# Performance work log

Hardware: AMD Instinct MI355X
Metric: run time of the kernel (lower is better)

## Reference

```python
import jax, jax.numpy as jnp
import numpy as np

N = 50000      # num nodes
E = 800000     # num edges
F_IN = 128     # CONFIG.FeatureLen()
H = 100        # conv1_hide
C = 16         # CONFIG.ClassNum()
LEAKY = 0.01


def setup_inputs() -> dict:
    key = jax.random.key(0)
    k = jax.random.split(key, 4)
    x = jax.random.normal(k[0], (N, F_IN), dtype=jnp.float32)
    edge_index = jax.random.randint(k[1], (2, E), 0, N, dtype=jnp.int32)
    W1 = jax.random.normal(k[2], (F_IN, H), dtype=jnp.float32) / np.sqrt(F_IN).astype(np.float32)
    b1 = jnp.zeros((H,), dtype=jnp.float32)
    W2 = jax.random.normal(k[3], (H, C), dtype=jnp.float32) / np.sqrt(H).astype(np.float32)
    b2 = jnp.zeros((C,), dtype=jnp.float32)
    return {"x": x, "W1": W1, "b1": b1, "W2": W2, "b2": b2, "edge_index": edge_index}


def _gcn_conv(x, W, b, src, dst):
    """PyG GCNConv: x' = D^{-1/2}(A+I)D^{-1/2} X W + b (symmetric norm, self-loops)."""
    x = x @ W  # transform first (smaller feature dim for propagation)
    loop = jnp.arange(N, dtype=src.dtype)
    s = jnp.concatenate([src, loop])  # sources (message senders)
    d = jnp.concatenate([dst, loop])  # targets (message receivers)
    deg = jax.ops.segment_sum(jnp.ones_like(d, dtype=x.dtype), d, num_segments=N)
    dinv = jnp.where(deg > 0, jax.lax.rsqrt(deg), 0.0)
    norm = dinv[s] * dinv[d]                      # [E+N]
    msg = x[s] * norm[:, None]                    # gather + scale
    out = jax.ops.segment_sum(msg, d, num_segments=N)  # scatter-add
    return out + b


def reference(x, W1, b1, W2, b2, edge_index):
    src, dst = edge_index[0], edge_index[1]
    h = _gcn_conv(x, W1, b1, src, dst)
    h = jax.nn.leaky_relu(h, negative_slope=LEAKY)
    # dropout is identity in eval mode (training=False)
    h = _gcn_conv(h, W2, b2, src, dst)
    return jax.nn.log_softmax(h, axis=1)
```

## Files before the change

kernel.cpp:

```cpp
#include <hip/hip_runtime.h>

#define F_IN 128
#define HDIM 100
#define HPAD 128
#define CDIM 16
#define CAP  64
#define BT_STRIDE 136
#define CHUNK 4096
#define KMAX 200
#define RCAP 64

static constexpr float LEAKY = 0.01f;

using short8  = __attribute__((ext_vector_type(8))) short;
using float4v = __attribute__((ext_vector_type(4))) float;
using float2v = __attribute__((ext_vector_type(2))) float;

__device__ __forceinline__ unsigned short f2bf(float f) {
    unsigned u = __float_as_uint(f);
    u += 0x7fffu + ((u >> 16) & 1u);
    return (unsigned short)(u >> 16);
}

__device__ __forceinline__ unsigned short f2h(float x) {
    union { unsigned short s; _Float16 f; } c;
    c.f = (_Float16)x;
    return c.s;
}

__device__ __forceinline__ float h2f(unsigned short u) {
    union { unsigned short s; _Float16 f; } c;
    c.s = u;
    return (float)c.f;
}


__global__ __launch_bounds__(256) void k_gemm1_p1(const float* __restrict__ x,
                                                  const float* __restrict__ W1,
                                                  unsigned char* __restrict__ y1f8,
                                                  const int* __restrict__ src,
                                                  const int* __restrict__ dst,
                                                  unsigned* __restrict__ bkt_edges,
                                                  int* __restrict__ cnt_arr,
                                                  int N, int E, int FB, int KBKT, int GB) {
    __shared__ union {
        unsigned short bt[F_IN * BT_STRIDE];
        struct { unsigned stage[CHUNK]; int cnt[KMAX]; } p1;
    } sm;
    int bx = blockIdx.x;
    int t = threadIdx.x;

    if (bx < FB) {
        unsigned* stage = sm.p1.stage;
        int* cnt = sm.p1.cnt;
        for (int i = t; i < KBKT; i += 256) cnt[i] = 0;
        __syncthreads();
        int e0 = bx * CHUNK, e1 = min(E, e0 + CHUNK);
        #pragma unroll 4
        for (int i = e0 + t; i < e1; i += 256) {
            int d = dst[i];
            unsigned pk = ((unsigned)d << 16) | (unsigned)src[i];
            atomicAdd(&cnt[d >> 8], 1);
            stage[i - e0] = pk;
        }
        __syncthreads();
        for (int i = t; i < KBKT; i += 256) cnt_arr[bx * KBKT + i] = cnt[i];
        __syncthreads();
        for (int i = t; i < KBKT; i += 256) cnt[i] = 0;
        __syncthreads();
        int m = e1 - e0;
        #pragma unroll 4
        for (int i = t; i < m; i += 256) {
            unsigned pk = stage[i];
            int b = pk >> 24;
            int pos = atomicAdd(&cnt[b], 1);
            if (pos < RCAP)
                bkt_edges[((size_t)b * FB + bx) * RCAP + pos] = pk;
        }
        return;
    }

    #pragma unroll 16
    for (int idx = t; idx < F_IN * HPAD; idx += 256) {
        int k = idx >> 7;
        int n = idx & 127;
        float v = (n < HDIM) ? W1[k * HDIM + n] : 0.f;
        sm.bt[n * BT_STRIDE + k] = f2bf(v);
    }
    __syncthreads();

    int wave = t >> 6, lane = t & 63;
    int Mtiles = (N + 15) >> 4;
    int m = lane & 15;
    int kq = lane >> 4;

    for (int tile = (bx - FB) * 4 + wave; tile < Mtiles; tile += 4 * GB) {
        int row0 = tile * 16;
        int arow = min(row0 + m, N - 1);
        const float* xrow = x + (size_t)arow * F_IN;

        short8 afrag[4];
        #pragma unroll
        for (int kt = 0; kt < 4; ++kt) {
            int kb = kt * 32 + kq * 8;
            float4 a0 = *(const float4*)(xrow + kb);
            float4 a1 = *(const float4*)(xrow + kb + 4);
            short8 f;
            f[0] = (short)f2bf(a0.x); f[1] = (short)f2bf(a0.y);
            f[2] = (short)f2bf(a0.z); f[3] = (short)f2bf(a0.w);
            f[4] = (short)f2bf(a1.x); f[5] = (short)f2bf(a1.y);
            f[6] = (short)f2bf(a1.z); f[7] = (short)f2bf(a1.w);
            afrag[kt] = f;
        }

        bool full = (row0 + 15 < N);
        #pragma unroll
        for (int ct = 0; ct < 8; ++ct) {
            float4v acc = {0.f, 0.f, 0.f, 0.f};
            #pragma unroll
            for (int kt = 0; kt < 4; ++kt) {
                short8 b = *(const short8*)&sm.bt[(ct * 16 + m) * BT_STRIDE + kt * 32 + kq * 8];
                acc = __builtin_amdgcn_mfma_f32_16x16x32_bf16(afrag[kt], b, acc, 0, 0, 0);
            }
            #pragma unroll
            for (int i = 0; i < 4; ++i) {
                int r = row0 + kq * 4 + i;
                int v8 = __builtin_amdgcn_cvt_pk_fp8_f32(acc[i], acc[i], 0, false);
                if (full || r < N)
                    y1f8[(size_t)r * HPAD + ct * 16 + m] = (unsigned char)(v8 & 0xff);
            }
        }
    }
}


__global__ __launch_bounds__(256) void k_p2(const unsigned* __restrict__ bkt_edges,
                                            const int* __restrict__ cnt_arr,
                                            int* __restrict__ deg,
                                            unsigned* __restrict__ slots,
                                            int N, int FB, int KBKT) {
    __shared__ int cur[256];
    int b = blockIdx.x, t = threadIdx.x;
    cur[t] = 0;
    __syncthreads();
    for (int fb = t; fb < FB; fb += 256) {
        int c = cnt_arr[fb * KBKT + b];
        size_t base = ((size_t)b * FB + fb) * RCAP;
        int j = 0;
        for (; j + 3 < c; j += 4) {
            uint4 pk4 = *(const uint4*)&bkt_edges[base + j];
            unsigned pks[4] = {pk4.x, pk4.y, pk4.z, pk4.w};
            #pragma unroll
            for (int q = 0; q < 4; ++q) {
                unsigned pk = pks[q];
                int d = pk >> 16;
                int pos = atomicAdd(&cur[d & 255], 1);
                if (pos < CAP)
                    slots[(size_t)d * CAP + pos] = pk & 0xffffu;
            }
        }
        for (; j < c; ++j) {
            unsigned pk = bkt_edges[base + j];
            int d = pk >> 16;
            int pos = atomicAdd(&cur[d & 255], 1);
            if (pos < CAP)
                slots[(size_t)d * CAP + pos] = pk & 0xffffu;
        }
    }
    __syncthreads();
    int n = (b << 8) + t;
    if (n < N) deg[n] = cur[t];
}


__global__ __launch_bounds__(256) void k_agg1y2(const unsigned* __restrict__ y1u,
                                                const float* __restrict__ b1,
                                                const float* __restrict__ W2,
                                                const int* __restrict__ deg,
                                                unsigned* __restrict__ slots,
                                                float* __restrict__ y2, int N) {
    __shared__ float W2s[HDIM * CDIM];
    __shared__ float hs[4][2][HPAD];
    int t = threadIdx.x;
    #pragma unroll 4
    for (int idx = t; idx < HDIM * CDIM; idx += 256) W2s[idx] = W2[idx];
    __syncthreads();

    int wave = t >> 6, lane = t & 63;
    int half = lane >> 5, l = lane & 31;
    int hbase = lane & 32;
    int n = blockIdx.x * 8 + wave * 2 + half;
    bool valid = (n < N);
    int nn = valid ? n : (N - 1);

    int beg = nn * CAP;
    int cnt = valid ? deg[nn] : 0;
    float dn = rsqrtf((float)deg[nn] + 1.0f);

    unsigned vn = y1u[(size_t)nn * 32 + l];
    float4 bb = (l < 25) ? *(const float4*)&b1[4 * l] : make_float4(0.f, 0.f, 0.f, 0.f);

    int cother = __shfl(cnt, lane ^ 32);
    int cmax = max(cnt, cother);

    float a0 = 0.f, a1 = 0.f, a2 = 0.f, a3 = 0.f;
    for (int e0 = 0; e0 < cmax; e0 += 32) {
        int mm = min(32, cnt - e0);
        unsigned su = 0u; float wv = 0.f;
        if (l < mm) {
            su = slots[beg + e0 + l] & 0xffffu;
            wv = rsqrtf((float)deg[su] + 1.0f);
            slots[beg + e0 + l] = su | ((unsigned)f2h(wv) << 16);
        }
        int mmax = min(32, cmax - e0);
        int mpad = (mmax + 15) & ~15;
        for (int j = 0; j < mpad; j += 16) {
            float w[16]; unsigned vv[16];
            #pragma unroll
            for (int q = 0; q < 16; ++q) {
                int ln = hbase | (j + q);
                unsigned s = (unsigned)__shfl((int)su, ln);
                w[q] = __shfl(wv, ln);
                vv[q] = y1u[(size_t)s * 32 + l];
            }
            #pragma unroll
            for (int q = 0; q < 16; ++q) {
                float2v lov = __builtin_amdgcn_cvt_pk_f32_fp8((int)vv[q], false);
                float2v hiv = __builtin_amdgcn_cvt_pk_f32_fp8((int)vv[q], true);
                a0 = fmaf(w[q], lov[0], a0);
                a1 = fmaf(w[q], lov[1], a1);
                a2 = fmaf(w[q], hiv[0], a2);
                a3 = fmaf(w[q], hiv[1], a3);
            }
        }
    }
    {
        float2v lov = __builtin_amdgcn_cvt_pk_f32_fp8((int)vn, false);
        float2v hiv = __builtin_amdgcn_cvt_pk_f32_fp8((int)vn, true);
        a0 = fmaf(dn, lov[0], a0);
        a1 = fmaf(dn, lov[1], a1);
        a2 = fmaf(dn, hiv[0], a2);
        a3 = fmaf(dn, hiv[1], a3);
    }

    float h0 = fmaf(dn, a0, bb.x);
    float h1 = fmaf(dn, a1, bb.y);
    float h2 = fmaf(dn, a2, bb.z);
    float h3 = fmaf(dn, a3, bb.w);
    h0 = h0 > 0.f ? h0 : LEAKY * h0;
    h1 = h1 > 0.f ? h1 : LEAKY * h1;
    h2 = h2 > 0.f ? h2 : LEAKY * h2;
    h3 = h3 > 0.f ? h3 : LEAKY * h3;
    *(float4*)&hs[wave][half][4 * l] = make_float4(h0, h1, h2, h3);
    __builtin_amdgcn_wave_barrier();

    int c = l & 15, kg = l >> 4;
    const float* hrow = hs[wave][half];
    float p = 0.f;
    #pragma unroll 10
    for (int j = 0; j < 50; ++j) {
        int k = 2 * j + kg;
        p = fmaf(hrow[k], W2s[k * CDIM + c], p);
    }
    p += __shfl_down(p, 16);
    if (l < 16 && valid) y2[(size_t)n * CDIM + c] = p;
}


__global__ __launch_bounds__(256) void k_agg2(const float* __restrict__ y2,
                                              const float* __restrict__ b2,
                                              const int* __restrict__ deg,
                                              const unsigned* __restrict__ slots,
                                              float* __restrict__ out, int N) {
    int t = threadIdx.x;
    int wave = t >> 6, lane = t & 63;
    int sub = lane >> 4, c = lane & 15;
    int n = blockIdx.x * 16 + wave * 4 + sub;
    bool valid = (n < N);
    int nn = valid ? n : 0;

    int beg = nn * CAP;
    int cnt = valid ? deg[nn] : 0;
    float dn = rsqrtf((float)deg[nn] + 1.0f);
    float acc = dn * y2[(size_t)nn * CDIM + c];

    for (int e0 = 0; e0 < cnt; e0 += 16) {
        int mm = min(16, cnt - e0);
        unsigned su = 0u; float wv = 0.f;
        if (c < mm) {
            unsigned sv = slots[beg + e0 + c];
            su = sv & 0xffffu;
            wv = h2f((unsigned short)(sv >> 16));
        }
        float w[16]; float v[16];
        #pragma unroll
        for (int q = 0; q < 16; ++q) {
            int ln = sub * 16 + q;
            unsigned s = (unsigned)__shfl((int)su, ln);
            w[q] = __shfl(wv, ln);
            v[q] = y2[(size_t)s * CDIM + c];
        }
        #pragma unroll
        for (int q = 0; q < 16; ++q) acc = fmaf(w[q], v[q], acc);
    }

    float lg = fmaf(dn, acc, b2[c]);
    float mx = lg;
    #pragma unroll
    for (int k = 8; k; k >>= 1) mx = fmaxf(mx, __shfl_xor(mx, k));
    float ex = __expf(lg - mx);
    #pragma unroll
    for (int k = 8; k; k >>= 1) ex += __shfl_xor(ex, k);
    float lse = mx + __logf(ex);
    if (valid) out[(size_t)n * CDIM + c] = lg - lse;
}


extern "C" void kernel_launch(void* const* d_in, const int* in_sizes, int n_in,
                              void* d_out, int out_size, void* d_ws, size_t ws_size,
                              hipStream_t stream) {
    const float* x  = (const float*)d_in[0];
    const float* W1 = (const float*)d_in[1];
    const float* b1 = (const float*)d_in[2];
    const float* W2 = (const float*)d_in[3];
    const float* b2 = (const float*)d_in[4];
    const int*   ei = (const int*)d_in[5];

    const int N = in_sizes[0] / F_IN;
    const int E = in_sizes[5] / 2;
    const int* src = ei;
    const int* dst = ei + E;

    const int KBKT = (N + 255) >> 8;
    const int FB   = (E + CHUNK - 1) / CHUNK;

    char* ws = (char*)d_ws;
    size_t off = 0;
    auto alloc = [&](size_t bytes) {
        char* p = ws + off;
        off += (bytes + 255) & ~(size_t)255;
        return p;
    };
    int*            deg       = (int*)alloc((size_t)N * 4);
    unsigned char*  y1f8      = (unsigned char*)alloc((size_t)N * HPAD);
    float*          y2        = (float*)alloc((size_t)N * CDIM * 4);
    unsigned*       slots     = (unsigned*)alloc((size_t)N * CAP * 4);
    int*            cnt_arr   = (int*)alloc((size_t)FB * KBKT * 4);
    unsigned*       bkt_edges = (unsigned*)alloc((size_t)KBKT * FB * RCAP * 4);
    (void)ws_size; (void)n_in; (void)out_size;

    const int GB = 262;

    k_gemm1_p1<<<FB + GB, 256, 0, stream>>>(x, W1, y1f8, src, dst,
                                            bkt_edges, cnt_arr, N, E, FB, KBKT, GB);
    k_p2<<<KBKT, 256, 0, stream>>>(bkt_edges, cnt_arr, deg, slots, N, FB, KBKT);
    k_agg1y2<<<(N + 7) / 8, 256, 0, stream>>>((const unsigned*)y1f8, b1, W2,
                                              deg, slots, y2, N);
    k_agg2<<<(N + 15) / 16, 256, 0, stream>>>(y2, b2, deg, slots,
                                              (float*)d_out, N);
}
```

Before: 158.9 us.

## Map one node per quarter-wave in layer-1 aggregation with two feature passes

The layer-1 aggregation kernel now assigns 16 lanes per node instead of 32, so each wave handles four nodes. Each lane covers the 128-byte fp8 row in two passes of 64 bytes. The second pass reuses the fp16 edge weight written into the slot array during the first pass rather than recomputing it. This aims to cut the lane waste and divergence that came from padding short neighbor lists to 16 within 32-lane halves, and it halves the grid size. The trade-off is narrower 64-byte gathers, edge lists read twice, fp16-rounded weights in the second pass, and a serial 100-step W2 dot product per lane.

```diff
diff --git a/kernel.cpp b/kernel.cpp
--- a/kernel.cpp
+++ b/kernel.cpp
@@ -180,16 +180,16 @@
                                                 unsigned* __restrict__ slots,
                                                 float* __restrict__ y2, int N) {
     __shared__ float W2s[HDIM * CDIM];
-    __shared__ float hs[4][2][HPAD];
+    __shared__ float hs[4][4][HPAD];
     int t = threadIdx.x;
     #pragma unroll 4
     for (int idx = t; idx < HDIM * CDIM; idx += 256) W2s[idx] = W2[idx];
     __syncthreads();
 
     int wave = t >> 6, lane = t & 63;
-    int half = lane >> 5, l = lane & 31;
-    int hbase = lane & 32;
-    int n = blockIdx.x * 8 + wave * 2 + half;
+    int quarter = lane >> 4, l2 = lane & 15;
+    int qbase = lane & 48;
+    int n = blockIdx.x * 16 + wave * 4 + quarter;
     bool valid = (n < N);
     int nn = valid ? n : (N - 1);
 
@@ -197,31 +197,32 @@
     int cnt = valid ? deg[nn] : 0;
     float dn = rsqrtf((float)deg[nn] + 1.0f);
 
-    unsigned vn = y1u[(size_t)nn * 32 + l];
-    float4 bb = (l < 25) ? *(const float4*)&b1[4 * l] : make_float4(0.f, 0.f, 0.f, 0.f);
-
-    int cother = __shfl(cnt, lane ^ 32);
-    int cmax = max(cnt, cother);
-
-    float a0 = 0.f, a1 = 0.f, a2 = 0.f, a3 = 0.f;
-    for (int e0 = 0; e0 < cmax; e0 += 32) {
-        int mm = min(32, cnt - e0);
-        unsigned su = 0u; float wv = 0.f;
-        if (l < mm) {
-            su = slots[beg + e0 + l] & 0xffffu;
-            wv = rsqrtf((float)deg[su] + 1.0f);
-            slots[beg + e0 + l] = su | ((unsigned)f2h(wv) << 16);
-        }
-        int mmax = min(32, cmax - e0);
-        int mpad = (mmax + 15) & ~15;
-        for (int j = 0; j < mpad; j += 16) {
+    unsigned vn0 = y1u[(size_t)nn * 32 + l2];
+    unsigned vn1 = y1u[(size_t)nn * 32 + 16 + l2];
+
+    #pragma unroll
+    for (int p = 0; p < 2; ++p) {
+        float a0 = 0.f, a1 = 0.f, a2 = 0.f, a3 = 0.f;
+        for (int e0 = 0; e0 < cnt; e0 += 16) {
+            int mm = min(16, cnt - e0);
+            unsigned su = 0u; float wv = 0.f;
+            if (l2 < mm) {
+                unsigned sv = slots[beg + e0 + l2];
+                su = sv & 0xffffu;
+                if (p == 0) {
+                    wv = rsqrtf((float)deg[su] + 1.0f);
+                    slots[beg + e0 + l2] = su | ((unsigned)f2h(wv) << 16);
+                } else {
+                    wv = h2f((unsigned short)(sv >> 16));
+                }
+            }
             float w[16]; unsigned vv[16];
             #pragma unroll
             for (int q = 0; q < 16; ++q) {
-                int ln = hbase | (j + q);
+                int ln = qbase | q;
                 unsigned s = (unsigned)__shfl((int)su, ln);
                 w[q] = __shfl(wv, ln);
-                vv[q] = y1u[(size_t)s * 32 + l];
+                vv[q] = y1u[(size_t)s * 32 + p * 16 + l2];
             }
             #pragma unroll
             for (int q = 0; q < 16; ++q) {
@@ -233,37 +234,36 @@
                 a3 = fmaf(w[q], hiv[1], a3);
             }
         }
-    }
-    {
-        float2v lov = __builtin_amdgcn_cvt_pk_f32_fp8((int)vn, false);
-        float2v hiv = __builtin_amdgcn_cvt_pk_f32_fp8((int)vn, true);
-        a0 = fmaf(dn, lov[0], a0);
-        a1 = fmaf(dn, lov[1], a1);
-        a2 = fmaf(dn, hiv[0], a2);
-        a3 = fmaf(dn, hiv[1], a3);
-    }
-
-    float h0 = fmaf(dn, a0, bb.x);
-    float h1 = fmaf(dn, a1, bb.y);
-    float h2 = fmaf(dn, a2, bb.z);
-    float h3 = fmaf(dn, a3, bb.w);
-    h0 = h0 > 0.f ? h0 : LEAKY * h0;
-    h1 = h1 > 0.f ? h1 : LEAKY * h1;
-    h2 = h2 > 0.f ? h2 : LEAKY * h2;
-    h3 = h3 > 0.f ? h3 : LEAKY * h3;
-    *(float4*)&hs[wave][half][4 * l] = make_float4(h0, h1, h2, h3);
+        {
+            unsigned vn = p ? vn1 : vn0;
+            float2v lov = __builtin_amdgcn_cvt_pk_f32_fp8((int)vn, false);
+            float2v hiv = __builtin_amdgcn_cvt_pk_f32_fp8((int)vn, true);
+            a0 = fmaf(dn, lov[0], a0);
+            a1 = fmaf(dn, lov[1], a1);
+            a2 = fmaf(dn, hiv[0], a2);
+            a3 = fmaf(dn, hiv[1], a3);
+        }
+
+        int f0 = p * 64 + 4 * l2;
+        float4 bb = (f0 < HDIM) ? *(const float4*)&b1[f0] : make_float4(0.f, 0.f, 0.f, 0.f);
+        float h0 = fmaf(dn, a0, bb.x);
+        float h1 = fmaf(dn, a1, bb.y);
+        float h2 = fmaf(dn, a2, bb.z);
+        float h3 = fmaf(dn, a3, bb.w);
+        h0 = h0 > 0.f ? h0 : LEAKY * h0;
+        h1 = h1 > 0.f ? h1 : LEAKY * h1;
+        h2 = h2 > 0.f ? h2 : LEAKY * h2;
+        h3 = h3 > 0.f ? h3 : LEAKY * h3;
+        *(float4*)&hs[wave][quarter][f0] = make_float4(h0, h1, h2, h3);
+    }
     __builtin_amdgcn_wave_barrier();
 
-    int c = l & 15, kg = l >> 4;
-    const float* hrow = hs[wave][half];
-    float p = 0.f;
+    const float* hrow = hs[wave][quarter];
+    float pacc = 0.f;
     #pragma unroll 10
-    for (int j = 0; j < 50; ++j) {
-        int k = 2 * j + kg;
-        p = fmaf(hrow[k], W2s[k * CDIM + c], p);
-    }
-    p += __shfl_down(p, 16);
-    if (l < 16 && valid) y2[(size_t)n * CDIM + c] = p;
+    for (int k = 0; k < HDIM; ++k)
+        pacc = fmaf(hrow[k], W2s[k * CDIM + l2], pacc);
+    if (valid) y2[(size_t)n * CDIM + l2] = pacc;
 }
 
 
@@ -354,8 +354,8 @@
     k_gemm1_p1<<<FB + GB, 256, 0, stream>>>(x, W1, y1f8, src, dst,
                                             bkt_edges, cnt_arr, N, E, FB, KBKT, GB);
     k_p2<<<KBKT, 256, 0, stream>>>(bkt_edges, cnt_arr, deg, slots, N, FB, KBKT);
-    k_agg1y2<<<(N + 7) / 8, 256, 0, stream>>>((const unsigned*)y1f8, b1, W2,
-                                              deg, slots, y2, N);
+    k_agg1y2<<<(N + 15) / 16, 256, 0, stream>>>((const unsigned*)y1f8, b1, W2,
+                                                deg, slots, y2, N);
     k_agg2<<<(N + 15) / 16, 256, 0, stream>>>(y2, b2, deg, slots,
                                               (float*)d_out, N);
 }
```

Result: no change. 161.8 us (+1.8%).

## Replace fixed-capacity per-node slots with compact CSR built via LDS staging and scans

Applied to the files above, without the earlier changes.

The per-node fixed-capacity (64) adjacency slot array becomes a compact CSR layout. k_p2 stages each bucket's edges into LDS, counts per-node degrees, prefix-scans them, and reserves a contiguous range through a global atomic cursor before scattering source ids. The aggregation kernels then read edge lists through an offset array. This shrinks the slots footprint and makes neighbour reads denser, at the cost of extra scans, syncs and one more indirection. Nodes come out in nondeterministic block order, and each bucket is capped at SCAP edges in staging.

```diff
diff --git a/kernel.cpp b/kernel.cpp
--- a/kernel.cpp
+++ b/kernel.cpp
@@ -4,11 +4,11 @@
 #define HDIM 100
 #define HPAD 128
 #define CDIM 16
-#define CAP  64
 #define BT_STRIDE 136
 #define CHUNK 4096
 #define KMAX 200
 #define RCAP 64
+#define SCAP 4608
 
 static constexpr float LEAKY = 0.01f;
 
@@ -42,6 +42,7 @@
                                                   const int* __restrict__ dst,
                                                   unsigned* __restrict__ bkt_edges,
                                                   int* __restrict__ cnt_arr,
+                                                  int* __restrict__ cursor,
                                                   int N, int E, int FB, int KBKT, int GB) {
     __shared__ union {
         unsigned short bt[F_IN * BT_STRIDE];
@@ -80,6 +81,7 @@
         return;
     }
 
+    if (bx == FB && t == 0) cursor[0] = 0;
     #pragma unroll 16
     for (int idx = t; idx < F_IN * HPAD; idx += 256) {
         int k = idx >> 7;
@@ -137,39 +139,79 @@
 __global__ __launch_bounds__(256) void k_p2(const unsigned* __restrict__ bkt_edges,
                                             const int* __restrict__ cnt_arr,
                                             int* __restrict__ deg,
+                                            int* __restrict__ off,
                                             unsigned* __restrict__ slots,
+                                            int* __restrict__ cursor,
                                             int N, int FB, int KBKT) {
+    __shared__ unsigned stage[SCAP];
+    __shared__ int tmp[256];
     __shared__ int cur[256];
+    __shared__ int nbase[256];
+    __shared__ int blkbase;
     int b = blockIdx.x, t = threadIdx.x;
+
+    int c = (t < FB) ? cnt_arr[t * KBKT + b] : 0;
+
+    tmp[t] = c; __syncthreads();
+    #pragma unroll
+    for (int s = 1; s < 256; s <<= 1) {
+        int v = (t >= s) ? tmp[t - s] : 0;
+        __syncthreads();
+        tmp[t] += v;
+        __syncthreads();
+    }
+    int sbase = tmp[t] - c;
+    int T = min(tmp[255], SCAP);
     cur[t] = 0;
     __syncthreads();
-    for (int fb = t; fb < FB; fb += 256) {
-        int c = cnt_arr[fb * KBKT + b];
-        size_t base = ((size_t)b * FB + fb) * RCAP;
+
+    if (c > 0) {
+        size_t base = ((size_t)b * FB + t) * RCAP;
+        int lim = min(c, SCAP - sbase);
         int j = 0;
-        for (; j + 3 < c; j += 4) {
+        for (; j + 3 < lim; j += 4) {
             uint4 pk4 = *(const uint4*)&bkt_edges[base + j];
-            unsigned pks[4] = {pk4.x, pk4.y, pk4.z, pk4.w};
-            #pragma unroll
-            for (int q = 0; q < 4; ++q) {
-                unsigned pk = pks[q];
-                int d = pk >> 16;
-                int pos = atomicAdd(&cur[d & 255], 1);
-                if (pos < CAP)
-                    slots[(size_t)d * CAP + pos] = pk & 0xffffu;
-            }
-        }
-        for (; j < c; ++j) {
-            unsigned pk = bkt_edges[base + j];
-            int d = pk >> 16;
-            int pos = atomicAdd(&cur[d & 255], 1);
-            if (pos < CAP)
-                slots[(size_t)d * CAP + pos] = pk & 0xffffu;
-        }
-    }
-    __syncthreads();
+            stage[sbase + j]     = pk4.x;
+            stage[sbase + j + 1] = pk4.y;
+            stage[sbase + j + 2] = pk4.z;
+            stage[sbase + j + 3] = pk4.w;
+        }
+        for (; j < lim; ++j) stage[sbase + j] = bkt_edges[base + j];
+    }
+    __syncthreads();
+
+    #pragma unroll 4
+    for (int i = t; i < T; i += 256)
+        atomicAdd(&cur[(stage[i] >> 16) & 255], 1);
+    __syncthreads();
+
+    int cv = cur[t];
+    tmp[t] = cv; __syncthreads();
+    #pragma unroll
+    for (int s = 1; s < 256; s <<= 1) {
+        int v = (t >= s) ? tmp[t - s] : 0;
+        __syncthreads();
+        tmp[t] += v;
+        __syncthreads();
+    }
+    nbase[t] = tmp[t] - cv;
+    if (t == 0) blkbase = atomicAdd(cursor, tmp[255]);
+    cur[t] = 0;
+    __syncthreads();
+
     int n = (b << 8) + t;
-    if (n < N) deg[n] = cur[t];
+    if (n < N) {
+        deg[n] = cv;
+        off[n] = blkbase + nbase[t];
+    }
+
+    #pragma unroll 4
+    for (int i = t; i < T; i += 256) {
+        unsigned pk = stage[i];
+        int dn = (pk >> 16) & 255;
+        int pos = atomicAdd(&cur[dn], 1);
+        slots[blkbase + nbase[dn] + pos] = pk & 0xffffu;
+    }
 }
 
 
@@ -177,6 +219,7 @@
                                                 const float* __restrict__ b1,
                                                 const float* __restrict__ W2,
                                                 const int* __restrict__ deg,
+                                                const int* __restrict__ off,
                                                 unsigned* __restrict__ slots,
                                                 float* __restrict__ y2, int N) {
     __shared__ float W2s[HDIM * CDIM];
@@ -193,7 +236,7 @@
     bool valid = (n < N);
     int nn = valid ? n : (N - 1);
 
-    int beg = nn * CAP;
+    int beg = off[nn];
     int cnt = valid ? deg[nn] : 0;
     float dn = rsqrtf((float)deg[nn] + 1.0f);
 
@@ -270,6 +313,7 @@
 __global__ __launch_bounds__(256) void k_agg2(const float* __restrict__ y2,
                                               const float* __restrict__ b2,
                                               const int* __restrict__ deg,
+                                              const int* __restrict__ off,
                                               const unsigned* __restrict__ slots,
                                               float* __restrict__ out, int N) {
     int t = threadIdx.x;
@@ -279,7 +323,7 @@
     bool valid = (n < N);
     int nn = valid ? n : 0;
 
-    int beg = nn * CAP;
+    int beg = off[nn];
     int cnt = valid ? deg[nn] : 0;
     float dn = rsqrtf((float)deg[nn] + 1.0f);
     float acc = dn * y2[(size_t)nn * CDIM + c];
@@ -335,27 +379,31 @@
     const int FB   = (E + CHUNK - 1) / CHUNK;
 
     char* ws = (char*)d_ws;
-    size_t off = 0;
+    size_t off0 = 0;
     auto alloc = [&](size_t bytes) {
-        char* p = ws + off;
-        off += (bytes + 255) & ~(size_t)255;
+        char* p = ws + off0;
+        off0 += (bytes + 255) & ~(size_t)255;
         return p;
     };
     int*            deg       = (int*)alloc((size_t)N * 4);
+    int*            off       = (int*)alloc((size_t)N * 4);
     unsigned char*  y1f8      = (unsigned char*)alloc((size_t)N * HPAD);
     float*          y2        = (float*)alloc((size_t)N * CDIM * 4);
-    unsigned*       slots     = (unsigned*)alloc((size_t)N * CAP * 4);
+    unsigned*       slots     = (unsigned*)alloc((size_t)E * 4 + 65536);
     int*            cnt_arr   = (int*)alloc((size_t)FB * KBKT * 4);
     unsigned*       bkt_edges = (unsigned*)alloc((size_t)KBKT * FB * RCAP * 4);
+    int*            cursor    = (int*)alloc(256);
     (void)ws_size; (void)n_in; (void)out_size;
 
     const int GB = 262;
 
     k_gemm1_p1<<<FB + GB, 256, 0, stream>>>(x, W1, y1f8, src, dst,
-                                            bkt_edges, cnt_arr, N, E, FB, KBKT, GB);
-    k_p2<<<KBKT, 256, 0, stream>>>(bkt_edges, cnt_arr, deg, slots, N, FB, KBKT);
+                                            bkt_edges, cnt_arr, cursor,
+                                            N, E, FB, KBKT, GB);
+    k_p2<<<KBKT, 256, 0, stream>>>(bkt_edges, cnt_arr, deg, off, slots, cursor,
+                                   N, FB, KBKT);
     k_agg1y2<<<(N + 7) / 8, 256, 0, stream>>>((const unsigned*)y1f8, b1, W2,
-                                              deg, slots, y2, N);
-    k_agg2<<<(N + 15) / 16, 256, 0, stream>>>(y2, b2, deg, slots,
+                                              deg, off, slots, y2, N);
+    k_agg2<<<(N + 15) / 16, 256, 0, stream>>>(y2, b2, deg, off, slots,
                                               (float*)d_out, N);
 }
```

New measurement: 161.2 us. No clear change (+1.4%).
